# Optimization experiments

Measured on AMD Instinct MI355X. Metric: run time of the kernel, lower is better.

The kernel has to match this reference:

```python
import jax, jax.numpy as jnp
import numpy as np

B, S, E, H = 2, 2048, 1024, 16
D = E // H  # head_dim = 64
FE = 4      # forward_expansion
EPS = 1e-5


def layernorm(x, g, b):
    mu = jnp.mean(x, axis=-1, keepdims=True)
    var = jnp.var(x, axis=-1, keepdims=True)
    return (x - mu) * jax.lax.rsqrt(var + EPS) * g + b


def setup_inputs() -> dict:
    key = jax.random.key(0)
    ks = jax.random.split(key, 16)
    s = lambda d: 1.0 / np.sqrt(d)
    return {
        "queries": jax.random.normal(ks[0], (B, S, E), jnp.float32),
        "keys": jax.random.normal(ks[1], (B, S, E), jnp.float32),
        "values": jax.random.normal(ks[2], (B, S, E), jnp.float32),
        "mask": jnp.ones((B, 1, S, S), jnp.int32),  # ignored (faithful to source bug)
        "Wq": jax.random.normal(ks[3], (D, D), jnp.float32) * s(D),
        "Wk": jax.random.normal(ks[4], (D, D), jnp.float32) * s(D),
        "Wv": jax.random.normal(ks[5], (D, D), jnp.float32) * s(D),
        "Wfc": jax.random.normal(ks[6], (E, E), jnp.float32) * s(E),
        "bfc": jnp.zeros((E,), jnp.float32),
        "W1": jax.random.normal(ks[7], (FE * E, E), jnp.float32) * s(E),
        "b1": jnp.zeros((FE * E,), jnp.float32),
        "W2": jax.random.normal(ks[8], (E, FE * E), jnp.float32) * s(FE * E),
        "b2": jnp.zeros((E,), jnp.float32),
        "ln1_g": jnp.ones((E,), jnp.float32),
        "ln1_b": jnp.zeros((E,), jnp.float32),
        "ln2_g": jnp.ones((E,), jnp.float32),
        "ln2_b": jnp.zeros((E,), jnp.float32),
    }


def reference(queries, keys, values, mask, Wq, Wk, Wv, Wfc, bfc, W1, b1, W2, b2,
              ln1_g, ln1_b, ln2_g, ln2_b):
    # --- MHA ---
    q = queries.reshape(B, S, H, D) @ Wq.T  # [B,S,H,D]
    k = keys.reshape(B, S, H, D) @ Wk.T
    v = values.reshape(B, S, H, D) @ Wv.T
    scores = jnp.einsum('bqhd,bkhd->bhqk', q, k)
    # source: softmax(scores / S**(-1/2)) == scores * sqrt(S)  (faithful quirk)
    # mask is ignored: source masked_fill is non-inplace and discarded
    attn = jax.nn.softmax(scores * jnp.sqrt(jnp.float32(S)), axis=-1)
    out = jnp.einsum('bhqk,bkhd->bqhd', attn, v).reshape(B, S, E)
    att = out @ Wfc.T + bfc
    # --- residual + LN + FFN + LN (dropout p=0 -> identity) ---
    h = layernorm(att + queries, ln1_g, ln1_b)
    x = jax.nn.relu(h @ W1.T + b1) @ W2.T + b2
    return layernorm(x + h, ln2_g, ln2_b)
```

## Files before the change

### kernel.cpp

```cpp
#include <hip/hip_runtime.h>
#include <hip/hip_bf16.h>
#include <math.h>

#define B_ 2
#define S_ 2048
#define E_ 1024
#define H_ 16
#define D_ 64
#define TOK (B_*S_)
#define SCALE 45.254833995939045f

typedef __bf16 bf16x8 __attribute__((ext_vector_type(8)));
typedef float floatx4 __attribute__((ext_vector_type(4)));
struct b4s { __hip_bfloat16 x, y, z, w; };

typedef const __attribute__((address_space(1))) char ga_char;
typedef __attribute__((address_space(3))) char ls_char;

__device__ __forceinline__ void gload_lds16(const void* g, ls_char* l) {
  __builtin_amdgcn_global_load_lds((ga_char*)g, l, 16, 0, 0);
}

#define SWZ(arr, half, row, qpos) \
  (*(bf16x8*)&arr[half][row][(((qpos) ^ ((row) & 3)) * 8)])

__global__ __launch_bounds__(256) void cast_f2b(
    const float* __restrict__ in, __hip_bfloat16* __restrict__ out, int n4) {
  int i = blockIdx.x * 256 + threadIdx.x;
  if (i < n4) {
    float4 v = ((const float4*)in)[i];
    b4s o;
    o.x = __float2bfloat16(v.x); o.y = __float2bfloat16(v.y);
    o.z = __float2bfloat16(v.z); o.w = __float2bfloat16(v.w);
    *(b4s*)(out + (size_t)i * 4) = o;
  }
}

__global__ __launch_bounds__(256) void cast_whl(
    const float* __restrict__ Wq, const float* __restrict__ Wk,
    const float* __restrict__ Wv, __hip_bfloat16* __restrict__ Whl) {
  const int idx = blockIdx.x * 256 + threadIdx.x;
  const int m = idx >> 10;
  const int off = (idx & 1023) * 4;
  const float* W = (m == 0) ? Wq : (m == 1) ? Wk : Wv;
  float4 v = *(const float4*)(W + off);
  b4s hi, lo;
  hi.x = __float2bfloat16(v.x); lo.x = __float2bfloat16(v.x - __bfloat162float(hi.x));
  hi.y = __float2bfloat16(v.y); lo.y = __float2bfloat16(v.y - __bfloat162float(hi.y));
  hi.z = __float2bfloat16(v.z); lo.z = __float2bfloat16(v.z - __bfloat162float(hi.z));
  hi.w = __float2bfloat16(v.w); lo.w = __float2bfloat16(v.w - __bfloat162float(hi.w));
  *(b4s*)(Whl + (size_t)m * 8192 + off) = hi;
  *(b4s*)(Whl + (size_t)m * 8192 + 4096 + off) = lo;
}

__global__ __launch_bounds__(256) void qkv_fused(
    const float* __restrict__ xq, const float* __restrict__ xk,
    const float* __restrict__ xv, const __hip_bfloat16* __restrict__ Whl,
    __hip_bfloat16* __restrict__ qhi, __hip_bfloat16* __restrict__ qlo,
    __hip_bfloat16* __restrict__ khi, __hip_bfloat16* __restrict__ klo,
    __hip_bfloat16* __restrict__ vt) {
  __shared__ __bf16 Xh[2][64][32], Xl[2][64][32];
  __shared__ __bf16 Vt[64][72];
  const int t = threadIdx.x, lane = t & 63, w = t >> 6;
  const int quad = lane >> 4, low = lane & 15;
  const int bh = blockIdx.y;
  const int b = bh >> 4, h = bh & 15;
  const int s0 = blockIdx.x * 64;
  const int sr = t >> 2;
  const int sc = (t & 3) * 16;
  const int scc = sc >> 5;
  const int p0 = (sc & 31) >> 3;

  for (int m = 0; m < 3; m++) {
    const float* xin = (m == 0) ? xq : (m == 1) ? xk : xv;
    const __hip_bfloat16* Wh = Whl + (size_t)m * 8192;
    const float sc_m = (m == 0) ? SCALE : 1.0f;

    __syncthreads();
    {
      const float* src = xin + ((size_t)(b * S_ + s0 + sr)) * E_ + h * 64 + sc;
      float4 f0 = *(const float4*)(src);
      float4 f1 = *(const float4*)(src + 4);
      float4 f2 = *(const float4*)(src + 8);
      float4 f3 = *(const float4*)(src + 12);
      float fv[16] = {f0.x, f0.y, f0.z, f0.w, f1.x, f1.y, f1.z, f1.w,
                      f2.x, f2.y, f2.z, f2.w, f3.x, f3.y, f3.z, f3.w};
      bf16x8 hi0, hi1, lo0, lo1;
      #pragma unroll
      for (int j = 0; j < 8; j++) {
        hi0[j] = (__bf16)fv[j];
        lo0[j] = (__bf16)(fv[j] - (float)hi0[j]);
        hi1[j] = (__bf16)fv[8 + j];
        lo1[j] = (__bf16)(fv[8 + j] - (float)hi1[j]);
      }
      SWZ(Xh, scc, sr, p0) = hi0;
      SWZ(Xh, scc, sr, p0 + 1) = hi1;
      SWZ(Xl, scc, sr, p0) = lo0;
      SWZ(Xl, scc, sr, p0 + 1) = lo1;
    }
    __syncthreads();

    bf16x8 ah[2], al[2];
    #pragma unroll
    for (int c = 0; c < 2; c++) {
      ah[c] = SWZ(Xh, c, w * 16 + low, quad);
      al[c] = SWZ(Xl, c, w * 16 + low, quad);
    }

    floatx4 acc[4];
    #pragma unroll
    for (int nn = 0; nn < 4; nn++) {
      floatx4 a = {};
      #pragma unroll
      for (int c = 0; c < 2; c++) {
        const __hip_bfloat16* wp = Wh + (nn * 16 + low) * 64 + c * 32 + quad * 8;
        bf16x8 wh_ = *(const bf16x8*)wp;
        bf16x8 wl_ = *(const bf16x8*)(wp + 4096);
        a = __builtin_amdgcn_mfma_f32_16x16x32_bf16(ah[c], wh_, a, 0, 0, 0);
        a = __builtin_amdgcn_mfma_f32_16x16x32_bf16(al[c], wh_, a, 0, 0, 0);
        a = __builtin_amdgcn_mfma_f32_16x16x32_bf16(ah[c], wl_, a, 0, 0, 0);
      }
      acc[nn] = a;
    }

    if (m < 2) {
      __hip_bfloat16* dh = (m == 0) ? qhi : khi;
      __hip_bfloat16* dl = (m == 0) ? qlo : klo;
      #pragma unroll
      for (int nn = 0; nn < 4; nn++) {
        #pragma unroll
        for (int i = 0; i < 4; i++) {
          const int s = s0 + w * 16 + quad * 4 + i;
          const int d = nn * 16 + low;
          const size_t adr = ((size_t)bh * S_ + s) * 64 + d;
          const float f = acc[nn][i] * sc_m;
          const __hip_bfloat16 hb = __float2bfloat16(f);
          dh[adr] = hb;
          dl[adr] = __float2bfloat16(f - __bfloat162float(hb));
        }
      }
    } else {
      #pragma unroll
      for (int nn = 0; nn < 4; nn++)
        #pragma unroll
        for (int i = 0; i < 4; i++)
          Vt[nn * 16 + low][w * 16 + quad * 4 + i] = (__bf16)acc[nn][i];
      __syncthreads();
      const int dr = t >> 2;
      const int scl = (t & 3) * 16;
      __hip_bfloat16* dst = vt + ((size_t)bh * 64 + dr) * S_ + s0 + scl;
      bf16x8 o0 = *(const bf16x8*)&Vt[dr][scl];
      bf16x8 o1 = *(const bf16x8*)&Vt[dr][scl + 8];
      *(bf16x8*)dst = o0;
      *(bf16x8*)(dst + 8) = o1;
    }
  }
}

__global__ __launch_bounds__(512, 4) void attn_mfma(
    const __hip_bfloat16* __restrict__ Qhi, const __hip_bfloat16* __restrict__ Qlo,
    const __hip_bfloat16* __restrict__ Khi, const __hip_bfloat16* __restrict__ Klo,
    const __hip_bfloat16* __restrict__ Vtg, __hip_bfloat16* __restrict__ ctx) {
  __shared__ __bf16 Kh[2][2][64][32], Kl[2][2][64][32], Vs[2][2][64][32];
  const int t = threadIdx.x, lane = t & 63, w = t >> 6;
  const int quad = lane >> 4, low = lane & 15;
  const int bh = blockIdx.y;
  const int qw = blockIdx.x * 128 + w * 16;

  const int sh = w >> 2;
  const int r0 = (w & 3) * 16;
  const int srow = r0 + (lane >> 2);
  const int sq = (lane & 3) ^ (srow & 3);
  const __hip_bfloat16* gK = Khi + ((size_t)bh * S_ + srow) * 64 + sh * 32 + sq * 8;
  const __hip_bfloat16* gL = Klo + ((size_t)bh * S_ + srow) * 64 + sh * 32 + sq * 8;
  const __hip_bfloat16* gV = Vtg + ((size_t)bh * 64 + srow) * S_ + sh * 32 + sq * 8;

  bf16x8 qh[2], ql[2];
  {
    const size_t qbase = ((size_t)bh * S_ + qw + low) * 64 + quad * 8;
    qh[0] = *(const bf16x8*)(Qhi + qbase);
    qh[1] = *(const bf16x8*)(Qhi + qbase + 32);
    ql[0] = *(const bf16x8*)(Qlo + qbase);
    ql[1] = *(const bf16x8*)(Qlo + qbase + 32);
  }

  floatx4 oacc[4] = {};
  float mrow = -3e38f, lrow = 0.f;

  gload_lds16(gK, (ls_char*)&Kh[0][sh][r0][0]);
  gload_lds16(gL, (ls_char*)&Kl[0][sh][r0][0]);
  gload_lds16(gV, (ls_char*)&Vs[0][sh][r0][0]);

  for (int kt = 0; kt < S_ / 64; kt++) {
    const int cur = kt & 1;
    __syncthreads();
    if (kt + 1 < S_ / 64) {
      gload_lds16(gK + (size_t)(kt + 1) * 4096, (ls_char*)&Kh[cur ^ 1][sh][r0][0]);
      gload_lds16(gL + (size_t)(kt + 1) * 4096, (ls_char*)&Kl[cur ^ 1][sh][r0][0]);
      gload_lds16(gV + (size_t)(kt + 1) * 64,   (ls_char*)&Vs[cur ^ 1][sh][r0][0]);
    }

    floatx4 sa[4];
    #pragma unroll
    for (int nn = 0; nn < 4; nn++) {
      const int prow = (nn & 1) * 32 + (nn >> 1) * 4 + (low >> 2) * 8 + (low & 3);
      bf16x8 kh0 = SWZ(Kh[cur], 0, prow, quad);
      bf16x8 kh1 = SWZ(Kh[cur], 1, prow, quad);
      bf16x8 kl0 = SWZ(Kl[cur], 0, prow, quad);
      bf16x8 kl1 = SWZ(Kl[cur], 1, prow, quad);
      floatx4 s = {};
      s = __builtin_amdgcn_mfma_f32_16x16x32_bf16(kh0, qh[0], s, 0, 0, 0);
      s = __builtin_amdgcn_mfma_f32_16x16x32_bf16(kh1, qh[1], s, 0, 0, 0);
      s = __builtin_amdgcn_mfma_f32_16x16x32_bf16(kl0, qh[0], s, 0, 0, 0);
      s = __builtin_amdgcn_mfma_f32_16x16x32_bf16(kl1, qh[1], s, 0, 0, 0);
      s = __builtin_amdgcn_mfma_f32_16x16x32_bf16(kh0, ql[0], s, 0, 0, 0);
      s = __builtin_amdgcn_mfma_f32_16x16x32_bf16(kh1, ql[1], s, 0, 0, 0);
      sa[nn] = s;
    }

    float rmax;
    {
      float m0 = fmaxf(fmaxf(sa[0][0], sa[0][1]), fmaxf(sa[0][2], sa[0][3]));
      float m1 = fmaxf(fmaxf(sa[1][0], sa[1][1]), fmaxf(sa[1][2], sa[1][3]));
      float m2 = fmaxf(fmaxf(sa[2][0], sa[2][1]), fmaxf(sa[2][2], sa[2][3]));
      float m3 = fmaxf(fmaxf(sa[3][0], sa[3][1]), fmaxf(sa[3][2], sa[3][3]));
      rmax = fmaxf(fmaxf(m0, m1), fmaxf(m2, m3));
      rmax = fmaxf(rmax, __shfl_xor(rmax, 16, 64));
      rmax = fmaxf(rmax, __shfl_xor(rmax, 32, 64));
    }
    if (__any(rmax > mrow)) {
      const float nm = fmaxf(mrow, rmax);
      const float al = __expf(mrow - nm);
      mrow = nm;
      lrow *= al;
      #pragma unroll
      for (int dt = 0; dt < 4; dt++) {
        oacc[dt][0] *= al; oacc[dt][1] *= al;
        oacc[dt][2] *= al; oacc[dt][3] *= al;
      }
    }
    float p[4][4];
    float rs;
    {
      float r0_ = 0.f, r1_ = 0.f, r2_ = 0.f, r3_ = 0.f;
      #pragma unroll
      for (int i = 0; i < 4; i++) {
        p[0][i] = __expf(sa[0][i] - mrow); r0_ += p[0][i];
        p[1][i] = __expf(sa[1][i] - mrow); r1_ += p[1][i];
        p[2][i] = __expf(sa[2][i] - mrow); r2_ += p[2][i];
        p[3][i] = __expf(sa[3][i] - mrow); r3_ += p[3][i];
      }
      rs = (r0_ + r1_) + (r2_ + r3_);
      rs += __shfl_xor(rs, 16, 64);
      rs += __shfl_xor(rs, 32, 64);
    }
    lrow += rs;

    bf16x8 pb[2];
    #pragma unroll
    for (int kh2 = 0; kh2 < 2; kh2++) {
      bf16x8 v;
      v[0] = (__bf16)p[kh2][0]; v[1] = (__bf16)p[kh2][1];
      v[2] = (__bf16)p[kh2][2]; v[3] = (__bf16)p[kh2][3];
      v[4] = (__bf16)p[kh2 + 2][0]; v[5] = (__bf16)p[kh2 + 2][1];
      v[6] = (__bf16)p[kh2 + 2][2]; v[7] = (__bf16)p[kh2 + 2][3];
      pb[kh2] = v;
    }

    #pragma unroll
    for (int dt = 0; dt < 4; dt++) {
      bf16x8 vb0 = SWZ(Vs[cur], 0, dt * 16 + low, quad);
      bf16x8 vb1 = SWZ(Vs[cur], 1, dt * 16 + low, quad);
      oacc[dt] = __builtin_amdgcn_mfma_f32_16x16x32_bf16(vb0, pb[0], oacc[dt], 0, 0, 0);
      oacc[dt] = __builtin_amdgcn_mfma_f32_16x16x32_bf16(vb1, pb[1], oacc[dt], 0, 0, 0);
    }
  }

  const float inv = 1.0f / lrow;
  const int b = bh >> 4, h = bh & 15;
  const size_t base = ((size_t)(b * S_ + qw + low)) * E_ + h * 64 + quad * 4;
  #pragma unroll
  for (int dt = 0; dt < 4; dt++) {
    b4s o;
    o.x = __float2bfloat16(oacc[dt][0] * inv);
    o.y = __float2bfloat16(oacc[dt][1] * inv);
    o.z = __float2bfloat16(oacc[dt][2] * inv);
    o.w = __float2bfloat16(oacc[dt][3] * inv);
    *(b4s*)(ctx + base + dt * 16) = o;
  }
}

template <int RELU, int OUT_BF16, int PARTIAL>
__global__ __launch_bounds__(256) void gemm_mfma(
    const __hip_bfloat16* __restrict__ A, const __hip_bfloat16* __restrict__ Wt,
    const float* __restrict__ bias, void* __restrict__ C0, void* __restrict__ C1,
    int M, int N, int Kblk, int lda) {
  __shared__ __bf16 As[128][32];
  __shared__ __bf16 Bs[128][32];
  const int t = threadIdx.x;
  const int lane = t & 63;
  const int w = t >> 6;
  const int wr = w >> 1, wc = w & 1;
  const int m0 = blockIdx.y * 128, n0 = blockIdx.x * 128;
  void* Cout = (blockIdx.z == 0) ? C0 : C1;

  A += (size_t)blockIdx.z * Kblk;
  Wt += (size_t)blockIdx.z * Kblk;

  floatx4 acc[4][4] = {};
  const int srow = t >> 2;
  const int schunk = (t & 3) * 8;

  const __hip_bfloat16* gA0 = A + (size_t)(m0 + srow) * lda + schunk;
  const __hip_bfloat16* gA1 = A + (size_t)(m0 + srow + 64) * lda + schunk;
  const __hip_bfloat16* gB0 = Wt + (size_t)(n0 + srow) * lda + schunk;
  const __hip_bfloat16* gB1 = Wt + (size_t)(n0 + srow + 64) * lda + schunk;
  ls_char* lA = (ls_char*)&As[0][0] + w * 1024;
  ls_char* lB = (ls_char*)&Bs[0][0] + w * 1024;

  for (int k0 = 0; k0 < Kblk; k0 += 32) {
    __syncthreads();
    gload_lds16(gA0 + k0, lA);
    gload_lds16(gA1 + k0, lA + 4096);
    gload_lds16(gB0 + k0, lB);
    gload_lds16(gB1 + k0, lB + 4096);
    __syncthreads();

    bf16x8 af[4], bf[4];
    #pragma unroll
    for (int i = 0; i < 4; i++) {
      af[i] = *(const bf16x8*)&As[wr * 64 + i * 16 + (lane & 15)][(lane >> 4) * 8];
      bf[i] = *(const bf16x8*)&Bs[wc * 64 + i * 16 + (lane & 15)][(lane >> 4) * 8];
    }
    #pragma unroll
    for (int mi = 0; mi < 4; mi++)
      #pragma unroll
      for (int ni = 0; ni < 4; ni++)
        acc[mi][ni] = __builtin_amdgcn_mfma_f32_16x16x32_bf16(
            af[mi], bf[ni], acc[mi][ni], 0, 0, 0);
  }

  const int cil = lane & 15;
  const int quad = lane >> 4;
  #pragma unroll
  for (int ni = 0; ni < 4; ni++) {
    const int col = n0 + wc * 64 + ni * 16 + cil;
    const float bb = PARTIAL ? 0.f : bias[col];
    #pragma unroll
    for (int mi = 0; mi < 4; mi++) {
      const int row = m0 + wr * 64 + mi * 16 + quad * 4;
      #pragma unroll
      for (int i = 0; i < 4; i++) {
        if (PARTIAL) {
          ((float*)Cout)[(size_t)(row + i) * N + col] = acc[mi][ni][i];
        } else {
          float vv = acc[mi][ni][i] + bb;
          if (RELU) vv = fmaxf(vv, 0.f);
          if (OUT_BF16)
            ((__hip_bfloat16*)Cout)[(size_t)(row + i) * N + col] = __float2bfloat16(vv);
          else
            ((float*)Cout)[(size_t)(row + i) * N + col] = vv;
        }
      }
    }
  }
}

template <int EMIT_BF16>
__global__ __launch_bounds__(256) void add_ln(
    const float* __restrict__ a0, const float* __restrict__ a1,
    const float* __restrict__ r, const float* __restrict__ bias,
    const float* __restrict__ g, const float* __restrict__ bt,
    float* __restrict__ out, __hip_bfloat16* __restrict__ outb) {
  __shared__ float red[16];
  const int tok = blockIdx.x, t = threadIdx.x;
  float4 av = ((const float4*)(a0 + (size_t)tok * E_))[t];
  float4 a2 = ((const float4*)(a1 + (size_t)tok * E_))[t];
  float4 rv = ((const float4*)(r + (size_t)tok * E_))[t];
  float4 cv = ((const float4*)bias)[t];
  float4 x;
  x.x = av.x + a2.x + rv.x + cv.x; x.y = av.y + a2.y + rv.y + cv.y;
  x.z = av.z + a2.z + rv.z + cv.z; x.w = av.w + a2.w + rv.w + cv.w;
  float sum = x.x + x.y + x.z + x.w;
  float ssq = x.x * x.x + x.y * x.y + x.z * x.z + x.w * x.w;
  #pragma unroll
  for (int off = 32; off >= 1; off >>= 1) {
    sum += __shfl_down(sum, off, 64);
    ssq += __shfl_down(ssq, off, 64);
  }
  const int wave = t >> 6;
  if ((t & 63) == 0) { red[wave] = sum; red[4 + wave] = ssq; }
  __syncthreads();
  if (t == 0) {
    float s = red[0] + red[1] + red[2] + red[3];
    float qq = red[4] + red[5] + red[6] + red[7];
    float mu = s * (1.0f / E_);
    red[8] = mu;
    red[9] = qq * (1.0f / E_) - mu * mu;
  }
  __syncthreads();
  const float mu = red[8];
  const float inv = rsqrtf(red[9] + 1e-5f);
  float4 gv = ((const float4*)g)[t];
  float4 bv = ((const float4*)bt)[t];
  float4 o;
  o.x = (x.x - mu) * inv * gv.x + bv.x;
  o.y = (x.y - mu) * inv * gv.y + bv.y;
  o.z = (x.z - mu) * inv * gv.z + bv.z;
  o.w = (x.w - mu) * inv * gv.w + bv.w;
  ((float4*)(out + (size_t)tok * E_))[t] = o;
  if (EMIT_BF16) {
    b4s ob;
    ob.x = __float2bfloat16(o.x); ob.y = __float2bfloat16(o.y);
    ob.z = __float2bfloat16(o.z); ob.w = __float2bfloat16(o.w);
    *(b4s*)(outb + (size_t)tok * E_ + t * 4) = ob;
  }
}

extern "C" void kernel_launch(void* const* d_in, const int* in_sizes, int n_in,
                              void* d_out, int out_size, void* d_ws, size_t ws_size,
                              hipStream_t stream) {
  const float* queries = (const float*)d_in[0];
  const float* keys    = (const float*)d_in[1];
  const float* values  = (const float*)d_in[2];
  const float* Wq  = (const float*)d_in[4];
  const float* Wk  = (const float*)d_in[5];
  const float* Wv  = (const float*)d_in[6];
  const float* Wfc = (const float*)d_in[7];
  const float* bfc = (const float*)d_in[8];
  const float* W1  = (const float*)d_in[9];
  const float* b1  = (const float*)d_in[10];
  const float* W2  = (const float*)d_in[11];
  const float* b2  = (const float*)d_in[12];
  const float* ln1_g = (const float*)d_in[13];
  const float* ln1_b = (const float*)d_in[14];
  const float* ln2_g = (const float*)d_in[15];
  const float* ln2_b = (const float*)d_in[16];

  const size_t M1 = 1048576;
  float* ws = (float*)d_ws;
  float* P0  = ws;
  float* P1  = ws + 4 * M1;
  float* Hf  = ws + 8 * M1;
  __hip_bfloat16* bb = (__hip_bfloat16*)(ws + 12 * M1);
  __hip_bfloat16* CTXb = bb;
  __hip_bfloat16* Hb   = bb + 4 * M1;
  __hip_bfloat16* Wfcb = bb + 8 * M1;
  __hip_bfloat16* W1b  = bb + 9 * M1;
  __hip_bfloat16* W2b  = bb + 13 * M1;
  __hip_bfloat16* Qhi  = bb + 17 * M1;
  __hip_bfloat16* Qlo  = bb + 21 * M1;
  __hip_bfloat16* Khi  = bb + 25 * M1;
  __hip_bfloat16* Klo  = bb + 29 * M1;
  __hip_bfloat16* Vtb  = bb + 33 * M1;
  __hip_bfloat16* FF1b = bb + 17 * M1;
  __hip_bfloat16* Whlb = bb + 37 * M1;
  float* out = (float*)d_out;

  cast_f2b<<<(E_ * E_ / 4 + 255) / 256, 256, 0, stream>>>(Wfc, Wfcb, E_ * E_ / 4);
  cast_f2b<<<(4 * E_ * E_ / 4 + 255) / 256, 256, 0, stream>>>(W1, W1b, 4 * E_ * E_ / 4);
  cast_f2b<<<(4 * E_ * E_ / 4 + 255) / 256, 256, 0, stream>>>(W2, W2b, 4 * E_ * E_ / 4);
  cast_whl<<<12, 256, 0, stream>>>(Wq, Wk, Wv, Whlb);

  qkv_fused<<<dim3(S_ / 64, B_ * H_), 256, 0, stream>>>(
      queries, keys, values, Whlb, Qhi, Qlo, Khi, Klo, Vtb);
  attn_mfma<<<dim3(S_ / 128, B_ * H_), 512, 0, stream>>>(
      Qhi, Qlo, Khi, Klo, Vtb, CTXb);
  gemm_mfma<0, 0, 1><<<dim3(E_ / 128, TOK / 128, 2), 256, 0, stream>>>(
      CTXb, Wfcb, nullptr, P0, P1, TOK, E_, 512, E_);
  add_ln<1><<<TOK, 256, 0, stream>>>(P0, P1, queries, bfc, ln1_g, ln1_b, Hf, Hb);
  gemm_mfma<1, 1, 0><<<dim3(4 * E_ / 128, TOK / 128, 1), 256, 0, stream>>>(
      Hb, W1b, b1, FF1b, FF1b, TOK, 4 * E_, E_, E_);
  gemm_mfma<0, 0, 1><<<dim3(E_ / 128, TOK / 128, 2), 256, 0, stream>>>(
      FF1b, W2b, nullptr, P0, P1, TOK, E_, 2048, 4 * E_);
  add_ln<0><<<TOK, 256, 0, stream>>>(P0, P1, Hf, b2, ln2_g, ln2_b, out, nullptr);
}
```

Baseline: 425.3 us.

## Merge weight casts, reorder attention grid, deepen GEMM K-tile with swizzled LDS

Folds the four weight-cast launches into a single kernel to cut launch overhead. Swaps the attention grid axes so consecutive blocks cover different heads rather than successive query tiles of the same head, which changes how blocks share K/V in cache. Doubles the GEMM K-step from 32 to 64 with an XOR-swizzled LDS layout, halving the number of barrier pairs per K and avoiding bank conflicts. The larger LDS tiles use more shared memory per block, which may reduce occupancy.

New measurement: 393.8 us. 1.08x faster.

```diff
diff --git a/kernel.cpp b/kernel.cpp
--- a/kernel.cpp
+++ b/kernel.cpp
@@ -24,33 +24,37 @@
 #define SWZ(arr, half, row, qpos) \
   (*(bf16x8*)&arr[half][row][(((qpos) ^ ((row) & 3)) * 8)])
 
-__global__ __launch_bounds__(256) void cast_f2b(
-    const float* __restrict__ in, __hip_bfloat16* __restrict__ out, int n4) {
-  int i = blockIdx.x * 256 + threadIdx.x;
-  if (i < n4) {
-    float4 v = ((const float4*)in)[i];
+__global__ __launch_bounds__(256) void cast_all(
+    const float* __restrict__ Wfc, const float* __restrict__ W1,
+    const float* __restrict__ W2, __hip_bfloat16* __restrict__ Wfcb,
+    __hip_bfloat16* __restrict__ W1b, __hip_bfloat16* __restrict__ W2b,
+    const float* __restrict__ Wq, const float* __restrict__ Wk,
+    const float* __restrict__ Wv, __hip_bfloat16* __restrict__ Whl) {
+  const int i = blockIdx.x * 256 + threadIdx.x;
+  if (i < 2359296) {
+    const float* src; __hip_bfloat16* dst; int j;
+    if (i < 262144)       { src = Wfc; dst = Wfcb; j = i; }
+    else if (i < 1310720) { src = W1;  dst = W1b;  j = i - 262144; }
+    else                  { src = W2;  dst = W2b;  j = i - 1310720; }
+    float4 v = ((const float4*)src)[j];
     b4s o;
     o.x = __float2bfloat16(v.x); o.y = __float2bfloat16(v.y);
     o.z = __float2bfloat16(v.z); o.w = __float2bfloat16(v.w);
-    *(b4s*)(out + (size_t)i * 4) = o;
-  }
-}
-
-__global__ __launch_bounds__(256) void cast_whl(
-    const float* __restrict__ Wq, const float* __restrict__ Wk,
-    const float* __restrict__ Wv, __hip_bfloat16* __restrict__ Whl) {
-  const int idx = blockIdx.x * 256 + threadIdx.x;
-  const int m = idx >> 10;
-  const int off = (idx & 1023) * 4;
-  const float* W = (m == 0) ? Wq : (m == 1) ? Wk : Wv;
-  float4 v = *(const float4*)(W + off);
-  b4s hi, lo;
-  hi.x = __float2bfloat16(v.x); lo.x = __float2bfloat16(v.x - __bfloat162float(hi.x));
-  hi.y = __float2bfloat16(v.y); lo.y = __float2bfloat16(v.y - __bfloat162float(hi.y));
-  hi.z = __float2bfloat16(v.z); lo.z = __float2bfloat16(v.z - __bfloat162float(hi.z));
-  hi.w = __float2bfloat16(v.w); lo.w = __float2bfloat16(v.w - __bfloat162float(hi.w));
-  *(b4s*)(Whl + (size_t)m * 8192 + off) = hi;
-  *(b4s*)(Whl + (size_t)m * 8192 + 4096 + off) = lo;
+    *(b4s*)(dst + (size_t)j * 4) = o;
+  } else if (i < 2362368) {
+    const int idx = i - 2359296;
+    const int m = idx >> 10;
+    const int off = (idx & 1023) * 4;
+    const float* W = (m == 0) ? Wq : (m == 1) ? Wk : Wv;
+    float4 v = *(const float4*)(W + off);
+    b4s hi, lo;
+    hi.x = __float2bfloat16(v.x); lo.x = __float2bfloat16(v.x - __bfloat162float(hi.x));
+    hi.y = __float2bfloat16(v.y); lo.y = __float2bfloat16(v.y - __bfloat162float(hi.y));
+    hi.z = __float2bfloat16(v.z); lo.z = __float2bfloat16(v.z - __bfloat162float(hi.z));
+    hi.w = __float2bfloat16(v.w); lo.w = __float2bfloat16(v.w - __bfloat162float(hi.w));
+    *(b4s*)(Whl + (size_t)m * 8192 + off) = hi;
+    *(b4s*)(Whl + (size_t)m * 8192 + 4096 + off) = lo;
+  }
 }
 
 __global__ __launch_bounds__(256) void qkv_fused(
@@ -164,8 +168,8 @@
   __shared__ __bf16 Kh[2][2][64][32], Kl[2][2][64][32], Vs[2][2][64][32];
   const int t = threadIdx.x, lane = t & 63, w = t >> 6;
   const int quad = lane >> 4, low = lane & 15;
-  const int bh = blockIdx.y;
-  const int qw = blockIdx.x * 128 + w * 16;
+  const int bh = blockIdx.x;
+  const int qw = blockIdx.y * 128 + w * 16;
 
   const int sh = w >> 2;
   const int r0 = (w & 3) * 16;
@@ -295,8 +299,8 @@
     const __hip_bfloat16* __restrict__ A, const __hip_bfloat16* __restrict__ Wt,
     const float* __restrict__ bias, void* __restrict__ C0, void* __restrict__ C1,
     int M, int N, int Kblk, int lda) {
-  __shared__ __bf16 As[128][32];
-  __shared__ __bf16 Bs[128][32];
+  __shared__ __bf16 As[128][64];
+  __shared__ __bf16 Bs[128][64];
   const int t = threadIdx.x;
   const int lane = t & 63;
   const int w = t >> 6;
@@ -308,36 +312,46 @@
   Wt += (size_t)blockIdx.z * Kblk;
 
   floatx4 acc[4][4] = {};
-  const int srow = t >> 2;
-  const int schunk = (t & 3) * 8;
-
-  const __hip_bfloat16* gA0 = A + (size_t)(m0 + srow) * lda + schunk;
-  const __hip_bfloat16* gA1 = A + (size_t)(m0 + srow + 64) * lda + schunk;
-  const __hip_bfloat16* gB0 = Wt + (size_t)(n0 + srow) * lda + schunk;
-  const __hip_bfloat16* gB1 = Wt + (size_t)(n0 + srow + 64) * lda + schunk;
+  const int srow = t >> 3;
+  const int ssc = ((t & 7) ^ (srow & 7)) * 8;
+
+  const __hip_bfloat16* gA = A + (size_t)(m0 + srow) * lda + ssc;
+  const __hip_bfloat16* gB = Wt + (size_t)(n0 + srow) * lda + ssc;
   ls_char* lA = (ls_char*)&As[0][0] + w * 1024;
   ls_char* lB = (ls_char*)&Bs[0][0] + w * 1024;
-
-  for (int k0 = 0; k0 < Kblk; k0 += 32) {
+  const size_t rstep = (size_t)32 * lda;
+
+  for (int k0 = 0; k0 < Kblk; k0 += 64) {
     __syncthreads();
-    gload_lds16(gA0 + k0, lA);
-    gload_lds16(gA1 + k0, lA + 4096);
-    gload_lds16(gB0 + k0, lB);
-    gload_lds16(gB1 + k0, lB + 4096);
+    gload_lds16(gA + k0,             lA);
+    gload_lds16(gA + k0 + rstep,     lA + 4096);
+    gload_lds16(gA + k0 + 2 * rstep, lA + 8192);
+    gload_lds16(gA + k0 + 3 * rstep, lA + 12288);
+    gload_lds16(gB + k0,             lB);
+    gload_lds16(gB + k0 + rstep,     lB + 4096);
+    gload_lds16(gB + k0 + 2 * rstep, lB + 8192);
+    gload_lds16(gB + k0 + 3 * rstep, lB + 12288);
     __syncthreads();
 
-    bf16x8 af[4], bf[4];
-    #pragma unroll
-    for (int i = 0; i < 4; i++) {
-      af[i] = *(const bf16x8*)&As[wr * 64 + i * 16 + (lane & 15)][(lane >> 4) * 8];
-      bf[i] = *(const bf16x8*)&Bs[wc * 64 + i * 16 + (lane & 15)][(lane >> 4) * 8];
-    }
-    #pragma unroll
-    for (int mi = 0; mi < 4; mi++)
-      #pragma unroll
-      for (int ni = 0; ni < 4; ni++)
-        acc[mi][ni] = __builtin_amdgcn_mfma_f32_16x16x32_bf16(
-            af[mi], bf[ni], acc[mi][ni], 0, 0, 0);
+    #pragma unroll
+    for (int ks = 0; ks < 2; ks++) {
+      bf16x8 af[4], bfr[4];
+      #pragma unroll
+      for (int i = 0; i < 4; i++) {
+        const int ra = wr * 64 + i * 16 + (lane & 15);
+        const int ca = (((lane >> 4) + ks * 4) ^ (ra & 7)) * 8;
+        af[i] = *(const bf16x8*)&As[ra][ca];
+        const int rb = wc * 64 + i * 16 + (lane & 15);
+        const int cb = (((lane >> 4) + ks * 4) ^ (rb & 7)) * 8;
+        bfr[i] = *(const bf16x8*)&Bs[rb][cb];
+      }
+      #pragma unroll
+      for (int mi = 0; mi < 4; mi++)
+        #pragma unroll
+        for (int ni = 0; ni < 4; ni++)
+          acc[mi][ni] = __builtin_amdgcn_mfma_f32_16x16x32_bf16(
+              af[mi], bfr[ni], acc[mi][ni], 0, 0, 0);
+    }
   }
 
   const int cil = lane & 15;
@@ -457,14 +471,12 @@
   __hip_bfloat16* Whlb = bb + 37 * M1;
   float* out = (float*)d_out;
 
-  cast_f2b<<<(E_ * E_ / 4 + 255) / 256, 256, 0, stream>>>(Wfc, Wfcb, E_ * E_ / 4);
-  cast_f2b<<<(4 * E_ * E_ / 4 + 255) / 256, 256, 0, stream>>>(W1, W1b, 4 * E_ * E_ / 4);
-  cast_f2b<<<(4 * E_ * E_ / 4 + 255) / 256, 256, 0, stream>>>(W2, W2b, 4 * E_ * E_ / 4);
-  cast_whl<<<12, 256, 0, stream>>>(Wq, Wk, Wv, Whlb);
+  cast_all<<<9228, 256, 0, stream>>>(Wfc, W1, W2, Wfcb, W1b, W2b,
+                                     Wq, Wk, Wv, Whlb);
 
   qkv_fused<<<dim3(S_ / 64, B_ * H_), 256, 0, stream>>>(
       queries, keys, values, Whlb, Qhi, Qlo, Khi, Klo, Vtb);
-  attn_mfma<<<dim3(S_ / 128, B_ * H_), 512, 0, stream>>>(
+  attn_mfma<<<dim3(B_ * H_, S_ / 128), 512, 0, stream>>>(
       Qhi, Qlo, Khi, Klo, Vtb, CTXb);
   gemm_mfma<0, 0, 1><<<dim3(E_ / 128, TOK / 128, 2), 256, 0, stream>>>(
       CTXb, Wfcb, nullptr, P0, P1, TOK, E_, 512, E_);
```
